# Kernel optimization log

Hardware: AMD Instinct MI355X
Metric: run time of the kernel (lower is better)

## Reference

```python
import jax, jax.numpy as jnp
import numpy as np

L, B, C, H = 1024, 8, 1024, 16
D = C // H  # 64


def setup_inputs() -> dict:
    key = jax.random.key(0)
    ks = jax.random.split(key, 8)
    hidden_states = jax.random.normal(ks[0], (L, B, C), dtype=jnp.float32)
    rotary_pos_emb = jax.random.uniform(ks[1], (L, D // 2), dtype=jnp.float32) * 10.0
    attention_mask = jax.random.randint(ks[2], (B, L, L), 0, 2) > 0
    s = 1.0 / np.sqrt(C)
    Wqkv = jax.random.uniform(ks[3], (3 * C, C), dtype=jnp.float32, minval=-s, maxval=s)
    bqkv = jax.random.uniform(ks[4], (3 * C,), dtype=jnp.float32, minval=-s, maxval=s)
    Wo = jax.random.uniform(ks[5], (C, C), dtype=jnp.float32, minval=-s, maxval=s)
    bo = jax.random.uniform(ks[6], (C,), dtype=jnp.float32, minval=-s, maxval=s)
    return {"hidden_states": hidden_states, "rotary_pos_emb": rotary_pos_emb,
            "attention_mask": attention_mask, "Wqkv": Wqkv, "bqkv": bqkv, "Wo": Wo, "bo": bo}


def _rotate_half(x):
    # interleaved pairs: [-x1, x0, -x3, x2, ...]
    x2 = x.reshape(*x.shape[:-1], -1, 2)
    return jnp.stack((-x2[..., 1], x2[..., 0]), axis=-1).reshape(x.shape)


def reference(hidden_states, rotary_pos_emb, attention_mask, Wqkv, bqkv, Wo, bo):
    Lx, Bx, Cx = hidden_states.shape
    # QKV projection: (L,B,3C) -> (3,B,L,H,D)
    qkv = hidden_states @ Wqkv.T + bqkv
    qkv = qkv.reshape(Lx, Bx, 3, H, D).transpose(2, 1, 0, 3, 4)
    q, k, v = qkv[0], qkv[1], qkv[2]  # (B, L, H, D)
    # RoPE: freqs (L, D/2) -> cos/sin (1, L, 1, D) via duplication
    rpe = rotary_pos_emb[None] if rotary_pos_emb.ndim == 2 else rotary_pos_emb
    cos = jnp.concatenate([jnp.cos(rpe), jnp.cos(rpe)], axis=-1)[:, :, None, :]
    sin = jnp.concatenate([jnp.sin(rpe), jnp.sin(rpe)], axis=-1)[:, :, None, :]
    q = q * cos + _rotate_half(q) * sin
    k = k * cos + _rotate_half(k) * sin
    # (B, H, L, D)
    q = q.transpose(0, 2, 1, 3)
    k = k.transpose(0, 2, 1, 3)
    v = v.transpose(0, 2, 1, 3)
    scale = 1.0 / jnp.sqrt(jnp.asarray(D, dtype=q.dtype))
    scores = jnp.einsum('bhqd,bhkd->bhqk', q, k) * scale
    # torch SDPA bool mask: True = attend, False = masked
    scores = jnp.where(attention_mask[:, None, :, :], scores, jnp.finfo(scores.dtype).min)
    attn = jax.nn.softmax(scores, axis=-1)
    out = jnp.einsum('bhqk,bhkd->bhqd', attn, v)  # (B, H, L, D)
    out = out.transpose(2, 0, 1, 3).reshape(Lx, Bx, Cx)  # (L, B, C)
    return out @ Wo.T + bo
```

## Files before the change

kernel.cpp:

```cpp
#include <hip/hip_runtime.h>
#include <hip/hip_bf16.h>

typedef short bf16x8 __attribute__((ext_vector_type(8)));
typedef short bf16x4 __attribute__((ext_vector_type(4)));
typedef float f32x4 __attribute__((ext_vector_type(4)));
typedef unsigned int u32;
typedef unsigned long long u64;

#define GLD_LDS16(gp, lp) \
  __builtin_amdgcn_global_load_lds((const __attribute__((address_space(1))) u32*)(gp), \
                                   (__attribute__((address_space(3))) u32*)(lp), 16, 0, 0)

__device__ __forceinline__ short f2bf(float f) {
  u32 u = __builtin_bit_cast(u32, f);
  u = (u + 0x7fffu + ((u >> 16) & 1u)) >> 16;
  return (short)u;
}

__device__ __forceinline__ u32 pack2_bf16(float a, float b) {
#if __has_builtin(__builtin_amdgcn_cvt_pk_bf16_f32)
  typedef __bf16 bf16v2 __attribute__((ext_vector_type(2)));
  bf16v2 r = __builtin_amdgcn_cvt_pk_bf16_f32(a, b);
  return __builtin_bit_cast(u32, r);
#else
  u32 r;
  asm("v_cvt_pk_bf16_f32 %0, %1, %2" : "=v"(r) : "v"(a), "v"(b));
  return r;
#endif
}

__device__ __forceinline__ float exp2_fast(float x) {
#if __has_builtin(__builtin_amdgcn_exp2f)
  return __builtin_amdgcn_exp2f(x);
#else
  return exp2f(x);
#endif
}

__device__ __forceinline__ u32 bytemask2(u32 src, u32 sel) {
  u32 r;
  asm("v_perm_b32 %0, %1, %1, %2" : "=v"(r) : "v"(src), "v"(sel));
  return r;
}

__global__ __launch_bounds__(256) void prep_all(
    const int* __restrict__ m, unsigned char* __restrict__ maskt,
    const float* __restrict__ hs, const float* __restrict__ wqkv,
    const float* __restrict__ wo, short* __restrict__ xb,
    short* __restrict__ wqkvb, short* __restrict__ wob,
    const float* __restrict__ rpe, float* __restrict__ cosT,
    float* __restrict__ sinT) {
  int b = blockIdx.x;
  if (b < 8192) {
    int i = b * 1024 + threadIdx.x * 4;
    int4 v = *(const int4*)(m + i);
    uchar4 o;
    o.x = v.x ? 0xFFu : 0u;
    o.y = v.y ? 0xFFu : 0u;
    o.z = v.z ? 0xFFu : 0u;
    o.w = v.w ? 0xFFu : 0u;
    *(uchar4*)(maskt + i) = o;
    return;
  }
  b -= 8192;
  if (b < 12288) {
    const float* in;
    short* out;
    int base;
    if (b < 8192) {
      in = hs; out = xb; base = b * 1024;
    } else if (b < 8192 + 3072) {
      in = wqkv; out = wqkvb; base = (b - 8192) * 1024;
    } else {
      in = wo; out = wob; base = (b - 11264) * 1024;
    }
    int i = base + threadIdx.x * 4;
    float4 v = *(const float4*)(in + i);
    short4 o;
    o.x = f2bf(v.x); o.y = f2bf(v.y); o.z = f2bf(v.z); o.w = f2bf(v.w);
    *(short4*)(out + i) = o;
    return;
  }
  b -= 12288;
  int i = b * 256 + threadIdx.x;
  float v = rpe[i];
  cosT[i] = cosf(v);
  sinT[i] = sinf(v);
}

__global__ __launch_bounds__(512, 2) void gemm_qkv(
    const short* __restrict__ Xb, const short* __restrict__ Wb,
    const float* __restrict__ bqkv, const float* __restrict__ cosT,
    const float* __restrict__ sinT, short* __restrict__ qb,
    short* __restrict__ kbuf, short* __restrict__ vbuf) {
  __shared__ short lds[3][24576];
  const int tid = threadIdx.x;
  const int wid = tid >> 6, lane = tid & 63;
  const int g = lane >> 4, c = lane & 15;
  const int wm = wid >> 2, wn = wid & 3;
  const int bid = blockIdx.y * 12 + blockIdx.x;
  const int swz = (bid & 7) * 96 + (bid >> 3);
  const int m0 = (swz / 12) * 128, n0 = (swz % 12) * 256;

  f32x4 acc[4][4];
#pragma unroll
  for (int i = 0; i < 4; i++)
#pragma unroll
    for (int j = 0; j < 4; j++) acc[i][j] = (f32x4){0.f, 0.f, 0.f, 0.f};

  const int trow = tid >> 3;
  const int gch = ((tid & 7) ^ (trow & 7)) * 8;
  const short* Ag = Xb + (long)(m0 + trow) * 1024 + gch;
  const short* Bg = Wb + (long)(n0 + trow) * 1024 + gch;
  const int lo = tid * 8;

  const int fA = (wm * 64 + c) * 64;
  const int fB = 8192 + (wn * 64 + c) * 64;
  const int ck0 = (g ^ (c & 7)) * 8;

#define QKV_STG(bs, ko) do { \
    GLD_LDS16(Ag + (ko),              &lds[bs][lo]); \
    GLD_LDS16(Ag + (ko) + 64 * 1024,  &lds[bs][4096 + lo]); \
    GLD_LDS16(Bg + (ko),              &lds[bs][8192 + lo]); \
    GLD_LDS16(Bg + (ko) + 64 * 1024,  &lds[bs][12288 + lo]); \
    GLD_LDS16(Bg + (ko) + 128 * 1024, &lds[bs][16384 + lo]); \
    GLD_LDS16(Bg + (ko) + 192 * 1024, &lds[bs][20480 + lo]); \
  } while (0)

  QKV_STG(0, 0);
  QKV_STG(1, 64);
  asm volatile("s_waitcnt vmcnt(6)" ::: "memory");
  __builtin_amdgcn_s_barrier();

  bf16x8 fa[2][4], fb[2][4];
#pragma unroll
  for (int mf = 0; mf < 4; mf++) fa[0][mf] = *(const bf16x8*)&lds[0][fA + mf * 1024 + ck0];
#pragma unroll
  for (int nf = 0; nf < 4; nf++) fb[0][nf] = *(const bf16x8*)&lds[0][fB + nf * 1024 + ck0];

#pragma unroll
  for (int kt = 0; kt < 16; ++kt) {
    const short* Bf = &lds[kt % 3][0];
#pragma unroll
    for (int mf = 0; mf < 4; mf++) fa[1][mf] = *(const bf16x8*)&Bf[fA + mf * 1024 + (ck0 ^ 32)];
#pragma unroll
    for (int nf = 0; nf < 4; nf++) fb[1][nf] = *(const bf16x8*)&Bf[fB + nf * 1024 + (ck0 ^ 32)];
    __builtin_amdgcn_sched_barrier(0);
    __builtin_amdgcn_s_setprio(1);
#pragma unroll
    for (int mf = 0; mf < 4; mf++)
#pragma unroll
      for (int nf = 0; nf < 4; nf++)
        acc[mf][nf] = __builtin_amdgcn_mfma_f32_16x16x32_bf16(fb[0][nf], fa[0][mf], acc[mf][nf], 0, 0, 0);
    __builtin_amdgcn_s_setprio(0);
    __builtin_amdgcn_sched_barrier(0);
    if (kt < 15) {
      asm volatile("s_waitcnt vmcnt(0)" ::: "memory");
      __builtin_amdgcn_s_barrier();
      if (kt < 14) QKV_STG((kt + 2) % 3, (kt + 2) * 64);
      const short* Bn = &lds[(kt + 1) % 3][0];
#pragma unroll
      for (int mf = 0; mf < 4; mf++) fa[0][mf] = *(const bf16x8*)&Bn[fA + mf * 1024 + ck0];
#pragma unroll
      for (int nf = 0; nf < 4; nf++) fb[0][nf] = *(const bf16x8*)&Bn[fB + nf * 1024 + ck0];
      __builtin_amdgcn_sched_barrier(0);
    }
    __builtin_amdgcn_s_setprio(1);
#pragma unroll
    for (int mf = 0; mf < 4; mf++)
#pragma unroll
      for (int nf = 0; nf < 4; nf++)
        acc[mf][nf] = __builtin_amdgcn_mfma_f32_16x16x32_bf16(fb[1][nf], fa[1][mf], acc[mf][nf], 0, 0, 0);
    __builtin_amdgcn_s_setprio(0);
  }
#undef QKV_STG

  for (int jt = 0; jt < 4; jt++) {
    const int chan = n0 + wn * 64 + jt * 16 + g * 4;
    const int three = chan >> 10;
    const int hh = (chan >> 6) & 15;
    const int d = chan & 63;
    const float4 bq = *(const float4*)&bqkv[chan];
    for (int i = 0; i < 4; i++) {
      const int r = m0 + wm * 64 + i * 16 + c;
      const int l = r >> 3, b = r & 7;
      float v0 = acc[i][jt][0] + bq.x;
      float v1 = acc[i][jt][1] + bq.y;
      float v2 = acc[i][jt][2] + bq.z;
      float v3 = acc[i][jt][3] + bq.w;
      const long doff = ((long)(b * 16 + hh) * 1024 + l) * 64 + d;
      if (three == 2) {
        uint2 o = {pack2_bf16(v0, v1), pack2_bf16(v2, v3)};
        *(uint2*)&vbuf[doff] = o;
      } else {
        const float4 cs = *(const float4*)&cosT[l * 32 + (d & 31)];
        const float4 sn = *(const float4*)&sinT[l * 32 + (d & 31)];
        float e0 = v0 * cs.x - v1 * sn.x;
        float o0 = v1 * cs.y + v0 * sn.y;
        float e1 = v2 * cs.z - v3 * sn.z;
        float o1 = v3 * cs.w + v2 * sn.w;
        short* dst;
        if (three == 0) {
          const float S = 0.18033688011f;
          e0 *= S; o0 *= S; e1 *= S; o1 *= S;
          dst = qb;
        } else {
          dst = kbuf;
        }
        uint2 o = {pack2_bf16(e0, o0), pack2_bf16(e1, o1)};
        *(uint2*)&dst[doff] = o;
      }
    }
  }
}

__global__ __launch_bounds__(256) void transpose_v(const short* __restrict__ vbuf,
                                                   short* __restrict__ vTb) {
  __shared__ short T[64 * 72];
  const int bh = blockIdx.y;
  const int l0 = blockIdx.x * 64;
  const int t = threadIdx.x;
  const int row = t >> 3;
  const int cc = (t & 7) * 8;
  const short* src = vbuf + ((long)bh * 1024 + l0) * 64;
  for (int p = 0; p < 2; p++) {
    int lr = row + p * 32;
    *(bf16x8*)&T[lr * 72 + cc] = *(const bf16x8*)&src[(long)lr * 64 + cc];
  }
  __syncthreads();
  short* dst = vTb + (long)bh * 64 * 1024 + l0;
  for (int p = 0; p < 2; p++) {
    int d = row + p * 32;
    bf16x8 v;
    for (int j = 0; j < 8; j++) v[j] = T[(cc + j) * 72 + d];
    *(bf16x8*)&dst[(long)d * 1024 + cc] = v;
  }
}

__global__ __launch_bounds__(256, 5) void flash_attn(
    const short* __restrict__ qb, const short* __restrict__ kbuf,
    const short* __restrict__ vTb, const unsigned char* __restrict__ maskt,
    short* __restrict__ attno) {
  __shared__ short K0[64 * 64], K1[64 * 64];
  __shared__ short V0[64 * 64], V1[64 * 64];
  const int t = threadIdx.x;
  const int wid = t >> 6, lane = t & 63;
  const int g = lane >> 4, c = lane & 15;
  const int bid = blockIdx.y * 16 + blockIdx.x;
  const int swz = (bid & 7) * 256 + (bid >> 3);
  const int q0 = (swz & 15) * 64;
  const int bh = swz >> 4;
  const int b = bh >> 4;
  const int h = bh & 15;
  const long qoff = (long)bh * 1024 * 64;
  const int qrow = q0 + wid * 16 + c;

  const u32 SEL01 = 0x01010000u;
  const u32 SEL23 = 0x03030202u;

  bf16x8 aq0, aq1;
  {
    const short* qp = qb + qoff + (long)qrow * 64;
    aq0 = *(const bf16x8*)(qp + g * 8);
    aq1 = *(const bf16x8*)(qp + 32 + g * 8);
  }

  f32x4 Od[4];
  for (int i = 0; i < 4; i++) Od[i] = (f32x4){0.f, 0.f, 0.f, 0.f};
  f32x4 Ld = (f32x4){0.f, 0.f, 0.f, 0.f};
  float m_run = -1e30f;

  bf16x8 avOnes8;
  {
    union { bf16x8 v; u32 u[4]; } av;
    u32 o1 = (c == 0) ? 0x3F803F80u : 0u;
    av.u[0] = av.u[1] = av.u[2] = av.u[3] = o1;
    avOnes8 = av.v;
  }

  const unsigned char* mrow8 = maskt + ((long)b * 1024 + qrow) * 1024 + g * 8;
  const short* Kg = kbuf + qoff;
  const short* Vg = vTb + qoff;

  const int l8 = lane >> 3, l7 = lane & 7;
  const int sr = wid * 16 + l8;
  const int sch = ((l7 ^ l8) & 7) * 8;
  const int r1 = wid * 16 + l8;
  const int r2 = r1 + 8;
  const int kp1 = (r1 & 32) | (((r1 & 15) >> 2) << 3) | (((r1 >> 4) & 1) << 2) | (r1 & 3);
  const int kp2 = (r2 & 32) | (((r2 & 15) >> 2) << 3) | (((r2 >> 4) & 1) << 2) | (r2 & 3);

  const int ck0 = g ^ (c & 7);
  const int kOff0 = c * 64 + ck0 * 8;
  const int kOff1 = c * 64 + (ck0 ^ 4) * 8;
  int vOff32[2];
  for (int kg = 0; kg < 2; kg++)
    vOff32[kg] = c * 64 + (((kg * 4 + g) ^ (c & 7)) * 8);

#define STAGE(KD, VD, ktn) do { \
    GLD_LDS16(Kg + (long)((ktn) + kp1) * 64 + sch,      &KD[(wid * 16) * 64]); \
    GLD_LDS16(Kg + (long)((ktn) + kp2) * 64 + sch,      &KD[(wid * 16 + 8) * 64]); \
    GLD_LDS16(Vg + (long)sr * 1024 + (ktn) + sch,       &VD[(wid * 16) * 64]); \
    GLD_LDS16(Vg + (long)(sr + 8) * 1024 + (ktn) + sch, &VD[(wid * 16 + 8) * 64]); \
  } while (0)

#define TILE(KB, VB, KP, VP, ki) do { \
    __syncthreads();  \
    STAGE(KP, VP, (((ki) + 1) & 15) * 64); \
     \
    const uint2 w0 = *(const uint2*)&mrow8[(ki) * 64]; \
    const uint2 w1 = *(const uint2*)&mrow8[(ki) * 64 + 32]; \
    f32x4 z[4]; \
    __builtin_amdgcn_s_setprio(1); \
    for (int nt = 0; nt < 4; nt++) { \
      bf16x8 bk0 = *(const bf16x8*)&KB[kOff0 + nt * 1024]; \
      bf16x8 bk1 = *(const bf16x8*)&KB[kOff1 + nt * 1024]; \
      f32x4 zz = (f32x4){0.f, 0.f, 0.f, 0.f}; \
      zz = __builtin_amdgcn_mfma_f32_16x16x32_bf16(bk0, aq0, zz, 0, 0, 0); \
      zz = __builtin_amdgcn_mfma_f32_16x16x32_bf16(bk1, aq1, zz, 0, 0, 0); \
      z[nt] = zz; \
    } \
    __builtin_amdgcn_s_setprio(0); \
    float mx = fmaxf(fmaxf(fmaxf(z[0][0], z[0][1]), fmaxf(z[0][2], z[0][3])), \
                     fmaxf(fmaxf(z[1][0], z[1][1]), fmaxf(z[1][2], z[1][3]))); \
    mx = fmaxf(mx, fmaxf(fmaxf(fmaxf(z[2][0], z[2][1]), fmaxf(z[2][2], z[2][3])), \
                         fmaxf(fmaxf(z[3][0], z[3][1]), fmaxf(z[3][2], z[3][3])))); \
    if (__ballot(mx > m_run + 8.f)) {  \
      mx = fmaxf(mx, __shfl_xor(mx, 16, 64)); \
      mx = fmaxf(mx, __shfl_xor(mx, 32, 64)); \
      float mnew = fmaxf(m_run, mx); \
      float al = exp2_fast(m_run - mnew); \
      for (int dt = 0; dt < 4; dt++) { \
        Od[dt][0] *= al; Od[dt][1] *= al; Od[dt][2] *= al; Od[dt][3] *= al; \
      } \
      Ld[0] *= al; \
      m_run = mnew; \
    } \
    union { bf16x8 v; u32 u[4]; } puA, puB; \
    { \
      float p0 = exp2_fast(z[0][0] - m_run), p1 = exp2_fast(z[0][1] - m_run); \
      float p2 = exp2_fast(z[0][2] - m_run), p3 = exp2_fast(z[0][3] - m_run); \
      float p4 = exp2_fast(z[1][0] - m_run), p5 = exp2_fast(z[1][1] - m_run); \
      float p6 = exp2_fast(z[1][2] - m_run), p7 = exp2_fast(z[1][3] - m_run); \
      puA.u[0] = pack2_bf16(p0, p1) & bytemask2(w0.x, SEL01); \
      puA.u[1] = pack2_bf16(p2, p3) & bytemask2(w0.x, SEL23); \
      puA.u[2] = pack2_bf16(p4, p5) & bytemask2(w0.y, SEL01); \
      puA.u[3] = pack2_bf16(p6, p7) & bytemask2(w0.y, SEL23); \
    } \
    { \
      float p0 = exp2_fast(z[2][0] - m_run), p1 = exp2_fast(z[2][1] - m_run); \
      float p2 = exp2_fast(z[2][2] - m_run), p3 = exp2_fast(z[2][3] - m_run); \
      float p4 = exp2_fast(z[3][0] - m_run), p5 = exp2_fast(z[3][1] - m_run); \
      float p6 = exp2_fast(z[3][2] - m_run), p7 = exp2_fast(z[3][3] - m_run); \
      puB.u[0] = pack2_bf16(p0, p1) & bytemask2(w1.x, SEL01); \
      puB.u[1] = pack2_bf16(p2, p3) & bytemask2(w1.x, SEL23); \
      puB.u[2] = pack2_bf16(p4, p5) & bytemask2(w1.y, SEL01); \
      puB.u[3] = pack2_bf16(p6, p7) & bytemask2(w1.y, SEL23); \
    } \
    __builtin_amdgcn_s_setprio(1); \
    Ld = __builtin_amdgcn_mfma_f32_16x16x32_bf16(avOnes8, puA.v, Ld, 0, 0, 0); \
    for (int dt = 0; dt < 4; dt++) { \
      bf16x8 av = *(const bf16x8*)&VB[vOff32[0] + dt * 1024]; \
      Od[dt] = __builtin_amdgcn_mfma_f32_16x16x32_bf16(av, puA.v, Od[dt], 0, 0, 0); \
    } \
    Ld = __builtin_amdgcn_mfma_f32_16x16x32_bf16(avOnes8, puB.v, Ld, 0, 0, 0); \
    for (int dt = 0; dt < 4; dt++) { \
      bf16x8 av = *(const bf16x8*)&VB[vOff32[1] + dt * 1024]; \
      Od[dt] = __builtin_amdgcn_mfma_f32_16x16x32_bf16(av, puB.v, Od[dt], 0, 0, 0); \
    } \
    __builtin_amdgcn_s_setprio(0); \
  } while (0)

  STAGE(K0, V0, 0);
  for (int ki = 0; ki < 16; ki += 2) {
    TILE(K0, V0, K1, V1, ki);
    TILE(K1, V1, K0, V0, ki + 1);
  }
#undef TILE
#undef STAGE

  float lsum = __shfl(Ld[0], c, 64);
  float inv = 1.f / lsum;
  long rbase = ((long)qrow * 8 + b) * 1024 + h * 64 + g * 4;
  for (int dt = 0; dt < 4; dt++) {
    union { bf16x4 v; u32 u[2]; } o;
    o.u[0] = pack2_bf16(Od[dt][0] * inv, Od[dt][1] * inv);
    o.u[1] = pack2_bf16(Od[dt][2] * inv, Od[dt][3] * inv);
    *(bf16x4*)&attno[rbase + dt * 16] = o.v;
  }
}

__global__ __launch_bounds__(256, 3) void gemm_out(
    const short* __restrict__ Ab, const short* __restrict__ Wob,
    const float* __restrict__ bo, float* __restrict__ out) {
  __shared__ short Ash[3][4096];
  __shared__ short Bsh[3][4096];
  const int tid = threadIdx.x;
  const int wid = tid >> 6, lane = tid & 63;
  const int g = lane >> 4, c = lane & 15;
  const int wm = wid >> 1, wn = wid & 1;
  const int bid = blockIdx.y * 8 + blockIdx.x;
  const int swz = (bid & 7) * 64 + (bid >> 3);
  const int m0 = (swz >> 3) * 128, n0 = (swz & 7) * 128;

  f32x4 acc[4][4];
#pragma unroll
  for (int i = 0; i < 4; i++)
#pragma unroll
    for (int j = 0; j < 4; j++) acc[i][j] = (f32x4){0.f, 0.f, 0.f, 0.f};

  const int srow = lane >> 2;
  const int scol = ((lane & 3) ^ ((lane >> 3) & 3)) * 8;
  const short* AgL = Ab + (long)(m0 + wid * 32 + srow) * 1024 + scol;
  const short* BgL = Wob + (long)(n0 + wid * 32 + srow) * 1024 + scol;
  const int dst0 = (wid * 32) * 32;
  const int dst1 = (wid * 32 + 16) * 32;
  const int ck = g ^ ((c >> 1) & 3);

#define OUT_STG(bs, ko) do { \
    GLD_LDS16(AgL + (ko), &Ash[bs][dst0]); \
    GLD_LDS16(AgL + (ko) + 16 * 1024, &Ash[bs][dst1]); \
    GLD_LDS16(BgL + (ko), &Bsh[bs][dst0]); \
    GLD_LDS16(BgL + (ko) + 16 * 1024, &Bsh[bs][dst1]); \
  } while (0)

  OUT_STG(0, 0);
  OUT_STG(1, 32);
  asm volatile("s_waitcnt vmcnt(4)" ::: "memory");
  __builtin_amdgcn_s_barrier();

  bf16x8 af[2][4], bfr[2][4];
#pragma unroll
  for (int i = 0; i < 4; i++)
    af[0][i] = *(const bf16x8*)&Ash[0][(wm * 64 + i * 16 + c) * 32 + ck * 8];
#pragma unroll
  for (int j = 0; j < 4; j++)
    bfr[0][j] = *(const bf16x8*)&Bsh[0][(wn * 64 + j * 16 + c) * 32 + ck * 8];

#pragma unroll
  for (int kt = 0; kt < 32; ++kt) {
    const int cur = kt & 1, nxt = cur ^ 1;
    __builtin_amdgcn_s_setprio(1);
#pragma unroll
    for (int i = 0; i < 2; i++)
#pragma unroll
      for (int j = 0; j < 4; j++)
        acc[i][j] = __builtin_amdgcn_mfma_f32_16x16x32_bf16(af[cur][i], bfr[cur][j], acc[i][j], 0, 0, 0);
    __builtin_amdgcn_s_setprio(0);
    __builtin_amdgcn_sched_barrier(0);
    if (kt < 31) {
      asm volatile("s_waitcnt vmcnt(0)" ::: "memory");
      __builtin_amdgcn_s_barrier();
      if (kt < 30) OUT_STG((kt + 2) % 3, (kt + 2) * 32);
      const int bn = (kt + 1) % 3;
#pragma unroll
      for (int i = 0; i < 4; i++)
        af[nxt][i] = *(const bf16x8*)&Ash[bn][(wm * 64 + i * 16 + c) * 32 + ck * 8];
#pragma unroll
      for (int j = 0; j < 4; j++)
        bfr[nxt][j] = *(const bf16x8*)&Bsh[bn][(wn * 64 + j * 16 + c) * 32 + ck * 8];
      __builtin_amdgcn_sched_barrier(0);
    }
    __builtin_amdgcn_s_setprio(1);
#pragma unroll
    for (int i = 2; i < 4; i++)
#pragma unroll
      for (int j = 0; j < 4; j++)
        acc[i][j] = __builtin_amdgcn_mfma_f32_16x16x32_bf16(af[cur][i], bfr[cur][j], acc[i][j], 0, 0, 0);
    __builtin_amdgcn_s_setprio(0);
  }
#undef OUT_STG

  for (int jt = 0; jt < 4; jt++) {
    const int j = n0 + wn * 64 + jt * 16 + c;
    const float bias = bo[j];
    for (int i = 0; i < 4; i++) {
      const int rbase = m0 + wm * 64 + i * 16 + g * 4;
      for (int reg = 0; reg < 4; reg++)
        out[(long)(rbase + reg) * 1024 + j] = acc[i][jt][reg] + bias;
    }
  }
}

extern "C" void kernel_launch(void* const* d_in, const int* in_sizes, int n_in,
                              void* d_out, int out_size, void* d_ws, size_t ws_size,
                              hipStream_t stream) {
  const float* hs = (const float*)d_in[0];
  const float* rpe = (const float*)d_in[1];
  const int* amask = (const int*)d_in[2];
  const float* Wqkv = (const float*)d_in[3];
  const float* bqkv = (const float*)d_in[4];
  const float* Wo = (const float*)d_in[5];
  const float* bo = (const float*)d_in[6];
  float* out = (float*)d_out;

  char* ws = (char*)d_ws;
  auto alloc = [&](size_t bytes) {
    char* p = ws;
    ws += (bytes + 255) & ~(size_t)255;
    return p;
  };
  short* Xb = (short*)alloc(8192LL * 1024 * 2);
  short* Wqkvb = (short*)alloc(3072LL * 1024 * 2);
  short* Wob = (short*)alloc(1024LL * 1024 * 2);
  float* cosT = (float*)alloc(1024 * 32 * 4);
  float* sinT = (float*)alloc(1024 * 32 * 4);
  unsigned char* maskt = (unsigned char*)alloc(8LL * 1024 * 1024);
  short* qb = (short*)alloc(128LL * 1024 * 64 * 2);
  short* kbuf = (short*)alloc(128LL * 1024 * 64 * 2);
  short* vbuf = (short*)alloc(128LL * 1024 * 64 * 2);
  short* vTb = (short*)alloc(128LL * 1024 * 64 * 2);
  short* attno = (short*)alloc(8192LL * 1024 * 2);

  prep_all<<<20608, 256, 0, stream>>>(amask, maskt, hs, Wqkv, Wo, Xb, Wqkvb, Wob,
                                      rpe, cosT, sinT);
  gemm_qkv<<<dim3(12, 64), 512, 0, stream>>>(Xb, Wqkvb, bqkv, cosT, sinT, qb, kbuf, vbuf);
  transpose_v<<<dim3(16, 128), 256, 0, stream>>>(vbuf, vTb);
  flash_attn<<<dim3(16, 128), 256, 0, stream>>>(qb, kbuf, vTb, maskt, attno);
  gemm_out<<<dim3(8, 64), 256, 0, stream>>>(attno, Wob, bo, out);
}
```

Baseline: 286.3 us.

## Restructure QKV and output GEMM pipelines to wait only for current stage

The QKV-projection and output-projection GEMM main loops are reorganised. Each iteration now waits with a partial vmcnt for just the current stage, issues a barrier, launches the prefetch two stages ahead, then loads all fragments from LDS and runs the MFMAs. The old register double-buffering of fragments, which interleaved LDS reads with MFMA halves and used a full vmcnt(0) wait, is removed. This keeps two global loads in flight across the barrier instead of draining them, but LDS read latency is no longer hidden behind MFMAs within a wave.

```diff
diff --git a/kernel.cpp b/kernel.cpp
--- a/kernel.cpp
+++ b/kernel.cpp
@@ -129,48 +129,38 @@
 
   QKV_STG(0, 0);
   QKV_STG(1, 64);
-  asm volatile("s_waitcnt vmcnt(6)" ::: "memory");
-  __builtin_amdgcn_s_barrier();
-
-  bf16x8 fa[2][4], fb[2][4];
-#pragma unroll
-  for (int mf = 0; mf < 4; mf++) fa[0][mf] = *(const bf16x8*)&lds[0][fA + mf * 1024 + ck0];
-#pragma unroll
-  for (int nf = 0; nf < 4; nf++) fb[0][nf] = *(const bf16x8*)&lds[0][fB + nf * 1024 + ck0];
 
 #pragma unroll
   for (int kt = 0; kt < 16; ++kt) {
+    if (kt < 15) {
+      asm volatile("s_waitcnt vmcnt(6)" ::: "memory");
+    } else {
+      asm volatile("s_waitcnt vmcnt(0)" ::: "memory");
+    }
+    __builtin_amdgcn_s_barrier();
+    __builtin_amdgcn_sched_barrier(0);
+    if (kt < 14) QKV_STG((kt + 2) % 3, (kt + 2) * 64);
     const short* Bf = &lds[kt % 3][0];
-#pragma unroll
-    for (int mf = 0; mf < 4; mf++) fa[1][mf] = *(const bf16x8*)&Bf[fA + mf * 1024 + (ck0 ^ 32)];
-#pragma unroll
-    for (int nf = 0; nf < 4; nf++) fb[1][nf] = *(const bf16x8*)&Bf[fB + nf * 1024 + (ck0 ^ 32)];
-    __builtin_amdgcn_sched_barrier(0);
+    bf16x8 fa0[4], fb0[4], fa1[4], fb1[4];
+#pragma unroll
+    for (int mf = 0; mf < 4; mf++) fa0[mf] = *(const bf16x8*)&Bf[fA + mf * 1024 + ck0];
+#pragma unroll
+    for (int nf = 0; nf < 4; nf++) fb0[nf] = *(const bf16x8*)&Bf[fB + nf * 1024 + ck0];
+#pragma unroll
+    for (int mf = 0; mf < 4; mf++) fa1[mf] = *(const bf16x8*)&Bf[fA + mf * 1024 + (ck0 ^ 32)];
+#pragma unroll
+    for (int nf = 0; nf < 4; nf++) fb1[nf] = *(const bf16x8*)&Bf[fB + nf * 1024 + (ck0 ^ 32)];
     __builtin_amdgcn_s_setprio(1);
 #pragma unroll
     for (int mf = 0; mf < 4; mf++)
 #pragma unroll
       for (int nf = 0; nf < 4; nf++)
-        acc[mf][nf] = __builtin_amdgcn_mfma_f32_16x16x32_bf16(fb[0][nf], fa[0][mf], acc[mf][nf], 0, 0, 0);
-    __builtin_amdgcn_s_setprio(0);
-    __builtin_amdgcn_sched_barrier(0);
-    if (kt < 15) {
-      asm volatile("s_waitcnt vmcnt(0)" ::: "memory");
-      __builtin_amdgcn_s_barrier();
-      if (kt < 14) QKV_STG((kt + 2) % 3, (kt + 2) * 64);
-      const short* Bn = &lds[(kt + 1) % 3][0];
-#pragma unroll
-      for (int mf = 0; mf < 4; mf++) fa[0][mf] = *(const bf16x8*)&Bn[fA + mf * 1024 + ck0];
-#pragma unroll
-      for (int nf = 0; nf < 4; nf++) fb[0][nf] = *(const bf16x8*)&Bn[fB + nf * 1024 + ck0];
-      __builtin_amdgcn_sched_barrier(0);
-    }
-    __builtin_amdgcn_s_setprio(1);
+        acc[mf][nf] = __builtin_amdgcn_mfma_f32_16x16x32_bf16(fb0[nf], fa0[mf], acc[mf][nf], 0, 0, 0);
 #pragma unroll
     for (int mf = 0; mf < 4; mf++)
 #pragma unroll
       for (int nf = 0; nf < 4; nf++)
-        acc[mf][nf] = __builtin_amdgcn_mfma_f32_16x16x32_bf16(fb[1][nf], fa[1][mf], acc[mf][nf], 0, 0, 0);
+        acc[mf][nf] = __builtin_amdgcn_mfma_f32_16x16x32_bf16(fb1[nf], fa1[mf], acc[mf][nf], 0, 0, 0);
     __builtin_amdgcn_s_setprio(0);
   }
 #undef QKV_STG
@@ -307,7 +297,6 @@
 #define TILE(KB, VB, KP, VP, ki) do { \
     __syncthreads();  \
     STAGE(KP, VP, (((ki) + 1) & 15) * 64); \
-     \
     const uint2 w0 = *(const uint2*)&mrow8[(ki) * 64]; \
     const uint2 w1 = *(const uint2*)&mrow8[(ki) * 64 + 32]; \
     f32x4 z[4]; \
@@ -426,47 +415,31 @@
 
   OUT_STG(0, 0);
   OUT_STG(1, 32);
-  asm volatile("s_waitcnt vmcnt(4)" ::: "memory");
-  __builtin_amdgcn_s_barrier();
-
-  bf16x8 af[2][4], bfr[2][4];
-#pragma unroll
-  for (int i = 0; i < 4; i++)
-    af[0][i] = *(const bf16x8*)&Ash[0][(wm * 64 + i * 16 + c) * 32 + ck * 8];
-#pragma unroll
-  for (int j = 0; j < 4; j++)
-    bfr[0][j] = *(const bf16x8*)&Bsh[0][(wn * 64 + j * 16 + c) * 32 + ck * 8];
 
 #pragma unroll
   for (int kt = 0; kt < 32; ++kt) {
-    const int cur = kt & 1, nxt = cur ^ 1;
+    if (kt < 31) {
+      asm volatile("s_waitcnt vmcnt(4)" ::: "memory");
+    } else {
+      asm volatile("s_waitcnt vmcnt(0)" ::: "memory");
+    }
+    __builtin_amdgcn_s_barrier();
+    __builtin_amdgcn_sched_barrier(0);
+    if (kt < 30) OUT_STG((kt + 2) % 3, (kt + 2) * 32);
+    const int bc = kt % 3;
+    bf16x8 af[4], bfr[4];
+#pragma unroll
+    for (int i = 0; i < 4; i++)
+      af[i] = *(const bf16x8*)&Ash[bc][(wm * 64 + i * 16 + c) * 32 + ck * 8];
+#pragma unroll
+    for (int j = 0; j < 4; j++)
+      bfr[j] = *(const bf16x8*)&Bsh[bc][(wn * 64 + j * 16 + c) * 32 + ck * 8];
     __builtin_amdgcn_s_setprio(1);
 #pragma unroll
-    for (int i = 0; i < 2; i++)
+    for (int i = 0; i < 4; i++)
 #pragma unroll
       for (int j = 0; j < 4; j++)
-        acc[i][j] = __builtin_amdgcn_mfma_f32_16x16x32_bf16(af[cur][i], bfr[cur][j], acc[i][j], 0, 0, 0);
-    __builtin_amdgcn_s_setprio(0);
-    __builtin_amdgcn_sched_barrier(0);
-    if (kt < 31) {
-      asm volatile("s_waitcnt vmcnt(0)" ::: "memory");
-      __builtin_amdgcn_s_barrier();
-      if (kt < 30) OUT_STG((kt + 2) % 3, (kt + 2) * 32);
-      const int bn = (kt + 1) % 3;
-#pragma unroll
-      for (int i = 0; i < 4; i++)
-        af[nxt][i] = *(const bf16x8*)&Ash[bn][(wm * 64 + i * 16 + c) * 32 + ck * 8];
-#pragma unroll
-      for (int j = 0; j < 4; j++)
-        bfr[nxt][j] = *(const bf16x8*)&Bsh[bn][(wn * 64 + j * 16 + c) * 32 + ck * 8];
-      __builtin_amdgcn_sched_barrier(0);
-    }
-    __builtin_amdgcn_s_setprio(1);
-#pragma unroll
-    for (int i = 2; i < 4; i++)
-#pragma unroll
-      for (int j = 0; j < 4; j++)
-        acc[i][j] = __builtin_amdgcn_mfma_f32_16x16x32_bf16(af[cur][i], bfr[cur][j], acc[i][j], 0, 0, 0);
+        acc[i][j] = __builtin_amdgcn_mfma_f32_16x16x32_bf16(af[i], bfr[j], acc[i][j], 0, 0, 0);
     __builtin_amdgcn_s_setprio(0);
   }
 #undef OUT_STG
```

Result: slower. 302.1 us (+5.5%).

## Double flash-attention query tile to 128 rows with 8 waves; restructure QKV GEMM pipeline

Applied to the files above, without the earlier changes.

Flash attention now launches 512-thread blocks, each covering 128 query rows, so every staged K/V tile in LDS is shared by eight waves instead of four. This halves the global K/V traffic per query and the number of staging loads per thread. The QKV GEMM loop is reorganised to wait on vmcnt(6) at the top of each k-step, issue the next prefetch, then load both k-halves from LDS before the MFMAs. That replaces the earlier software-pipelined register double-buffering and the vmcnt(0) wait. The trade-off is less overlap between LDS reads and MFMAs in the GEMM, plus higher register pressure per CU at launch bounds (512, 8) in attention.

```diff
diff --git a/kernel.cpp b/kernel.cpp
--- a/kernel.cpp
+++ b/kernel.cpp
@@ -129,48 +129,38 @@
 
   QKV_STG(0, 0);
   QKV_STG(1, 64);
-  asm volatile("s_waitcnt vmcnt(6)" ::: "memory");
-  __builtin_amdgcn_s_barrier();
-
-  bf16x8 fa[2][4], fb[2][4];
-#pragma unroll
-  for (int mf = 0; mf < 4; mf++) fa[0][mf] = *(const bf16x8*)&lds[0][fA + mf * 1024 + ck0];
-#pragma unroll
-  for (int nf = 0; nf < 4; nf++) fb[0][nf] = *(const bf16x8*)&lds[0][fB + nf * 1024 + ck0];
 
 #pragma unroll
   for (int kt = 0; kt < 16; ++kt) {
+    if (kt < 15) {
+      asm volatile("s_waitcnt vmcnt(6)" ::: "memory");
+    } else {
+      asm volatile("s_waitcnt vmcnt(0)" ::: "memory");
+    }
+    __builtin_amdgcn_s_barrier();
+    __builtin_amdgcn_sched_barrier(0);
+    if (kt < 14) QKV_STG((kt + 2) % 3, (kt + 2) * 64);
     const short* Bf = &lds[kt % 3][0];
-#pragma unroll
-    for (int mf = 0; mf < 4; mf++) fa[1][mf] = *(const bf16x8*)&Bf[fA + mf * 1024 + (ck0 ^ 32)];
-#pragma unroll
-    for (int nf = 0; nf < 4; nf++) fb[1][nf] = *(const bf16x8*)&Bf[fB + nf * 1024 + (ck0 ^ 32)];
-    __builtin_amdgcn_sched_barrier(0);
+    bf16x8 fa0[4], fb0[4], fa1[4], fb1[4];
+#pragma unroll
+    for (int mf = 0; mf < 4; mf++) fa0[mf] = *(const bf16x8*)&Bf[fA + mf * 1024 + ck0];
+#pragma unroll
+    for (int nf = 0; nf < 4; nf++) fb0[nf] = *(const bf16x8*)&Bf[fB + nf * 1024 + ck0];
+#pragma unroll
+    for (int mf = 0; mf < 4; mf++) fa1[mf] = *(const bf16x8*)&Bf[fA + mf * 1024 + (ck0 ^ 32)];
+#pragma unroll
+    for (int nf = 0; nf < 4; nf++) fb1[nf] = *(const bf16x8*)&Bf[fB + nf * 1024 + (ck0 ^ 32)];
     __builtin_amdgcn_s_setprio(1);
 #pragma unroll
     for (int mf = 0; mf < 4; mf++)
 #pragma unroll
       for (int nf = 0; nf < 4; nf++)
-        acc[mf][nf] = __builtin_amdgcn_mfma_f32_16x16x32_bf16(fb[0][nf], fa[0][mf], acc[mf][nf], 0, 0, 0);
-    __builtin_amdgcn_s_setprio(0);
-    __builtin_amdgcn_sched_barrier(0);
-    if (kt < 15) {
-      asm volatile("s_waitcnt vmcnt(0)" ::: "memory");
-      __builtin_amdgcn_s_barrier();
-      if (kt < 14) QKV_STG((kt + 2) % 3, (kt + 2) * 64);
-      const short* Bn = &lds[(kt + 1) % 3][0];
-#pragma unroll
-      for (int mf = 0; mf < 4; mf++) fa[0][mf] = *(const bf16x8*)&Bn[fA + mf * 1024 + ck0];
-#pragma unroll
-      for (int nf = 0; nf < 4; nf++) fb[0][nf] = *(const bf16x8*)&Bn[fB + nf * 1024 + ck0];
-      __builtin_amdgcn_sched_barrier(0);
-    }
-    __builtin_amdgcn_s_setprio(1);
+        acc[mf][nf] = __builtin_amdgcn_mfma_f32_16x16x32_bf16(fb0[nf], fa0[mf], acc[mf][nf], 0, 0, 0);
 #pragma unroll
     for (int mf = 0; mf < 4; mf++)
 #pragma unroll
       for (int nf = 0; nf < 4; nf++)
-        acc[mf][nf] = __builtin_amdgcn_mfma_f32_16x16x32_bf16(fb[1][nf], fa[1][mf], acc[mf][nf], 0, 0, 0);
+        acc[mf][nf] = __builtin_amdgcn_mfma_f32_16x16x32_bf16(fb1[nf], fa1[mf], acc[mf][nf], 0, 0, 0);
     __builtin_amdgcn_s_setprio(0);
   }
 #undef QKV_STG
@@ -237,7 +227,7 @@
   }
 }
 
-__global__ __launch_bounds__(256, 5) void flash_attn(
+__global__ __launch_bounds__(512, 8) void flash_attn(
     const short* __restrict__ qb, const short* __restrict__ kbuf,
     const short* __restrict__ vTb, const unsigned char* __restrict__ maskt,
     short* __restrict__ attno) {
@@ -246,10 +236,10 @@
   const int t = threadIdx.x;
   const int wid = t >> 6, lane = t & 63;
   const int g = lane >> 4, c = lane & 15;
-  const int bid = blockIdx.y * 16 + blockIdx.x;
-  const int swz = (bid & 7) * 256 + (bid >> 3);
-  const int q0 = (swz & 15) * 64;
-  const int bh = swz >> 4;
+  const int bid = blockIdx.y * 8 + blockIdx.x;
+  const int swz = (bid & 7) * 128 + (bid >> 3);
+  const int q0 = (swz & 7) * 128;
+  const int bh = swz >> 3;
   const int b = bh >> 4;
   const int h = bh & 15;
   const long qoff = (long)bh * 1024 * 64;
@@ -282,13 +272,10 @@
   const short* Kg = kbuf + qoff;
   const short* Vg = vTb + qoff;
 
-  const int l8 = lane >> 3, l7 = lane & 7;
-  const int sr = wid * 16 + l8;
-  const int sch = ((l7 ^ l8) & 7) * 8;
-  const int r1 = wid * 16 + l8;
-  const int r2 = r1 + 8;
-  const int kp1 = (r1 & 32) | (((r1 & 15) >> 2) << 3) | (((r1 >> 4) & 1) << 2) | (r1 & 3);
-  const int kp2 = (r2 & 32) | (((r2 & 15) >> 2) << 3) | (((r2 >> 4) & 1) << 2) | (r2 & 3);
+  const int rr = t >> 3;
+  const int sch = (((t & 7) ^ (rr & 7)) & 7) * 8;
+  const int kp = (rr & 32) | (((rr & 15) >> 2) << 3) | (((rr >> 4) & 1) << 2) | (rr & 3);
+  const int ldsb = (wid * 8) * 64;
 
   const int ck0 = g ^ (c & 7);
   const int kOff0 = c * 64 + ck0 * 8;
@@ -298,16 +285,13 @@
     vOff32[kg] = c * 64 + (((kg * 4 + g) ^ (c & 7)) * 8);
 
 #define STAGE(KD, VD, ktn) do { \
-    GLD_LDS16(Kg + (long)((ktn) + kp1) * 64 + sch,      &KD[(wid * 16) * 64]); \
-    GLD_LDS16(Kg + (long)((ktn) + kp2) * 64 + sch,      &KD[(wid * 16 + 8) * 64]); \
-    GLD_LDS16(Vg + (long)sr * 1024 + (ktn) + sch,       &VD[(wid * 16) * 64]); \
-    GLD_LDS16(Vg + (long)(sr + 8) * 1024 + (ktn) + sch, &VD[(wid * 16 + 8) * 64]); \
+    GLD_LDS16(Kg + (long)((ktn) + kp) * 64 + sch, &KD[ldsb]); \
+    GLD_LDS16(Vg + (long)rr * 1024 + (ktn) + sch, &VD[ldsb]); \
   } while (0)
 
 #define TILE(KB, VB, KP, VP, ki) do { \
     __syncthreads();  \
     STAGE(KP, VP, (((ki) + 1) & 15) * 64); \
-     \
     const uint2 w0 = *(const uint2*)&mrow8[(ki) * 64]; \
     const uint2 w1 = *(const uint2*)&mrow8[(ki) * 64 + 32]; \
     f32x4 z[4]; \
@@ -516,6 +500,6 @@
                                       rpe, cosT, sinT);
   gemm_qkv<<<dim3(12, 64), 512, 0, stream>>>(Xb, Wqkvb, bqkv, cosT, sinT, qb, kbuf, vbuf);
   transpose_v<<<dim3(16, 128), 256, 0, stream>>>(vbuf, vTb);
-  flash_attn<<<dim3(16, 128), 256, 0, stream>>>(qb, kbuf, vTb, maskt, attno);
+  flash_attn<<<dim3(8, 128), 512, 0, stream>>>(qb, kbuf, vTb, maskt, attno);
   gemm_out<<<dim3(8, 64), 256, 0, stream>>>(attno, Wob, bo, out);
 }
```

New measurement: 468.1 us. +63.5%, slower.
